# Kernel tuning notes

Measured on AMD Instinct MI355X. Metric: run time of the kernel, lower is better.

## Reference

```python
import jax, jax.numpy as jnp
import numpy as np

SEQ, BATCH, HID, NLAYERS = 2048, 16, 1024, 2


def setup_inputs() -> dict:
    key = jax.random.key(0)
    ks = jax.random.split(key, 3)
    scale = 1.0 / np.sqrt(HID)
    x = jax.random.normal(ks[0], (SEQ, BATCH, HID), dtype=jnp.float32)
    W0 = jax.random.normal(ks[1], (HID, 3 * HID), dtype=jnp.float32) * scale
    b0 = jnp.zeros((2 * HID,), dtype=jnp.float32)
    W1 = jax.random.normal(ks[2], (HID, 3 * HID), dtype=jnp.float32) * scale
    b1 = jnp.zeros((2 * HID,), dtype=jnp.float32)
    return {"x": x, "W0": W0, "b0": b0, "W1": W1, "b1": b1}


def _sru_layer(x, W, b):
    # x: [L, B, H]; W: [H, 3H]; b: [2H]
    L, B, H = x.shape
    U = jnp.einsum('lbd,dk->lbk', x, W)  # [L, B, 3H]
    x_tilde = U[..., :H]
    bf, br = b[:H], b[H:]
    f = jax.nn.sigmoid(U[..., H:2 * H] + bf)  # forget gate [L,B,H]
    r = jax.nn.sigmoid(U[..., 2 * H:] + br)   # reset gate  [L,B,H]

    def step(c_prev, inp):
        xt_t, f_t = inp
        c_t = f_t * c_prev + (1.0 - f_t) * xt_t
        return c_t, c_t

    c0 = jnp.zeros((B, H), dtype=x.dtype)
    _, cs = jax.lax.scan(step, c0, (x_tilde, f))  # cs: [L, B, H]
    h = r * cs + (1.0 - r) * x  # highway connection
    return h


def reference(x, W0, b0, W1, b1):
    h = _sru_layer(x, W0, b0)
    h = _sru_layer(h, W1, b1)
    return h[-1:]  # [1, B, H], matching `out[-1:]`
```

## Files before the change

kernel.cpp:

```cpp
#include <hip/hip_runtime.h>

#define SEQ    2048
#define BATCH  16
#define HID    1024
#define M_TOT  (SEQ*BATCH)
#define NCH    (BATCH*HID)
#define NCHUNK 64
#define TCHUNK (SEQ/NCHUNK)
#define NSEG   256

typedef __attribute__((ext_vector_type(8))) short          short8;
typedef __attribute__((ext_vector_type(8))) unsigned short ushort8_t;
typedef __attribute__((ext_vector_type(4))) float          floatx4;

__device__ __forceinline__ unsigned short f32_to_bf16(float f) {
  unsigned int u = __float_as_uint(f);
  u += 0x7FFFu + ((u >> 16) & 1u);
  return (unsigned short)(u >> 16);
}
__device__ __forceinline__ float bf16_to_f32(unsigned short h) {
  return __uint_as_float(((unsigned int)h) << 16);
}
__device__ __forceinline__ float sigmoidf_(float x) {
  return 1.f / (1.f + __expf(-x));
}


__device__ __forceinline__ void cast_swizzle_body(const float* __restrict__ src,
    unsigned short* __restrict__ dst, int mt, int kt, int t) {
  __shared__ unsigned short tile[4096];
  const int r = t >> 1, kh = (t & 1) * 16;
  const float* sp = src + (size_t)(mt * 128 + r) * 1024 + kt * 32 + kh;
  float4 v0 = *(const float4*)(sp + 0);
  float4 v1 = *(const float4*)(sp + 4);
  float4 v2 = *(const float4*)(sp + 8);
  float4 v3 = *(const float4*)(sp + 12);
  ushort8_t u0, u1;
  u0[0]=f32_to_bf16(v0.x); u0[1]=f32_to_bf16(v0.y); u0[2]=f32_to_bf16(v0.z); u0[3]=f32_to_bf16(v0.w);
  u0[4]=f32_to_bf16(v1.x); u0[5]=f32_to_bf16(v1.y); u0[6]=f32_to_bf16(v1.z); u0[7]=f32_to_bf16(v1.w);
  u1[0]=f32_to_bf16(v2.x); u1[1]=f32_to_bf16(v2.y); u1[2]=f32_to_bf16(v2.z); u1[3]=f32_to_bf16(v2.w);
  u1[4]=f32_to_bf16(v3.x); u1[5]=f32_to_bf16(v3.y); u1[6]=f32_to_bf16(v3.z); u1[7]=f32_to_bf16(v3.w);
  const int c = r >> 4, lr = r & 15, q0 = kh >> 3;
  const int unit0 = c * 64 + (q0 << 4) + lr;
  *(ushort8_t*)&tile[unit0 * 8]        = u0;
  *(ushort8_t*)&tile[(unit0 + 16) * 8] = u1;
  __syncthreads();
  const size_t base = ((size_t)mt * 32 + kt) * 4096;
  *(ushort8_t*)&dst[base + t * 16]     = *(const ushort8_t*)&tile[t * 16];
  *(ushort8_t*)&dst[base + t * 16 + 8] = *(const ushort8_t*)&tile[t * 16 + 8];
}

__device__ __forceinline__ void w_prep_body(const float* __restrict__ W,
    unsigned short* __restrict__ Wsw, int nt, int kt, int t) {
  __shared__ unsigned short tile[4096];
  const int kk = t >> 3, n0 = (t & 7) * 16;
  const float* sp = W + (size_t)(kt * 32 + kk) * 3072 + nt * 128 + n0;
  float v[16];
#pragma unroll
  for (int i = 0; i < 16; i += 4) {
    float4 f = *(const float4*)(sp + i);
    v[i] = f.x; v[i+1] = f.y; v[i+2] = f.z; v[i+3] = f.w;
  }
  const int cbase = (n0 >> 4) * 64 + ((kk >> 3) << 4);
#pragma unroll
  for (int j = 0; j < 16; j++)
    tile[(cbase + j) * 8 + (kk & 7)] = f32_to_bf16(v[j]);
  __syncthreads();
  const size_t base = ((size_t)nt * 32 + kt) * 4096;
  *(ushort8_t*)&Wsw[base + t * 16]     = *(const ushort8_t*)&tile[t * 16];
  *(ushort8_t*)&Wsw[base + t * 16 + 8] = *(const ushort8_t*)&tile[t * 16 + 8];
}

__global__ __launch_bounds__(256) void prep_all(const float* __restrict__ x,
    const float* __restrict__ W0, const float* __restrict__ W1,
    unsigned short* __restrict__ xsw, unsigned short* __restrict__ W0sw,
    unsigned short* __restrict__ W1sw) {
  const int id = blockIdx.x, t = threadIdx.x;
  if (id < 8192)        cast_swizzle_body(x, xsw, id >> 5, id & 31, t);
  else if (id < 8960)   w_prep_body(W0, W0sw, (id - 8192) >> 5, (id - 8192) & 31, t);
  else                  w_prep_body(W1, W1sw, (id - 8960) >> 5, (id - 8960) & 31, t);
}

typedef __attribute__((address_space(1))) const unsigned int GUI;
typedef __attribute__((address_space(3))) unsigned int LUI;
__device__ __forceinline__ void gl16(const unsigned short* g, unsigned short* l) {
  __builtin_amdgcn_global_load_lds((GUI*)g, (LUI*)l, 16, 0, 0);
}
__device__ __forceinline__ void barrier_fence() {
  asm volatile("s_barrier" ::: "memory");
}

__global__ __launch_bounds__(512, 2) void gemm_pipe(
    const unsigned short* __restrict__ A, const unsigned short* __restrict__ B,
    unsigned short* __restrict__ Xt, unsigned short* __restrict__ Fo,
    unsigned short* __restrict__ Ro, const float* __restrict__ bias)
{
  __shared__ unsigned short lds[65536];
  const int tid = threadIdx.x;
  const int wave = tid >> 6, lane = tid & 63;
  const int wm = wave >> 2, wn = wave & 3;
  const int id = blockIdx.x;
  const int xcd = id & 7, slot = id >> 3;
  const int g = slot / 96, r = slot % 96;
  const int bn = r >> 3;
  const int bm = xcd * 16 + g * 8 + (r & 7);

  const unsigned short* aSrc0 = A + ((size_t)(2 * bm + 0) * 32) * 4096 + tid * 8;
  const unsigned short* aSrc1 = A + ((size_t)(2 * bm + 1) * 32) * 4096 + tid * 8;
  const unsigned short* bSrc0 = B + ((size_t)(2 * bn + 0) * 32) * 4096 + tid * 8;
  const unsigned short* bSrc1 = B + ((size_t)(2 * bn + 1) * 32) * 4096 + tid * 8;

  floatx4 acc[8][4];
#pragma unroll
  for (int i = 0; i < 8; i++)
#pragma unroll
    for (int j = 0; j < 4; j++)
#pragma unroll
      for (int rr = 0; rr < 4; rr++) acc[i][j][rr] = 0.f;

#pragma unroll
  for (int u = 0; u < 3; ++u) {
    unsigned short* d = &lds[u * 16384 + wave * 512];
    gl16(aSrc0 + (size_t)u * 4096, d);
    gl16(aSrc1 + (size_t)u * 4096, d + 4096);
    gl16(bSrc0 + (size_t)u * 4096, d + 8192);
    gl16(bSrc1 + (size_t)u * 4096, d + 12288);
  }
  asm volatile("s_waitcnt vmcnt(0)" ::: "memory");
  barrier_fence();

  const int aoff = wm * 4096 + lane * 8;
  const int boff = 8192 + (wn >> 1) * 4096 + (wn & 1) * 2048 + lane * 8;

#pragma unroll 1
  for (int t = 0; t < 32; ++t) {
    const int sb = (t & 3) * 16384;
    const int u = t + 3;
    const unsigned short* As = &lds[sb + aoff];
    const unsigned short* Bs = &lds[sb + boff];
    short8 br[4], ar[4];
#pragma unroll
    for (int nj = 0; nj < 4; ++nj) br[nj] = *(const short8*)(Bs + nj * 512);
#pragma unroll
    for (int mi = 0; mi < 4; ++mi) ar[mi] = *(const short8*)(As + mi * 512);
    if (u < 32) {
      unsigned short* d = &lds[(u & 3) * 16384 + wave * 512];
      gl16(aSrc0 + (size_t)u * 4096, d);
      gl16(aSrc1 + (size_t)u * 4096, d + 4096);
    }
    __builtin_amdgcn_s_setprio(1);
#pragma unroll
    for (int mi = 0; mi < 4; ++mi)
#pragma unroll
      for (int nj = 0; nj < 4; ++nj)
        acc[mi][nj] = __builtin_amdgcn_mfma_f32_16x16x32_bf16(ar[mi], br[nj], acc[mi][nj], 0, 0, 0);
    __builtin_amdgcn_s_setprio(0);
#pragma unroll
    for (int mi = 0; mi < 4; ++mi) ar[mi] = *(const short8*)(As + (4 + mi) * 512);
    if (u < 32) {
      unsigned short* d = &lds[(u & 3) * 16384 + 8192 + wave * 512];
      gl16(bSrc0 + (size_t)u * 4096, d);
      gl16(bSrc1 + (size_t)u * 4096, d + 4096);
    }
    __builtin_amdgcn_s_setprio(1);
#pragma unroll
    for (int mi = 0; mi < 4; ++mi)
#pragma unroll
      for (int nj = 0; nj < 4; ++nj)
        acc[4 + mi][nj] = __builtin_amdgcn_mfma_f32_16x16x32_bf16(ar[mi], br[nj], acc[4 + mi][nj], 0, 0, 0);
    __builtin_amdgcn_s_setprio(0);
    if (t <= 28)      asm volatile("s_waitcnt vmcnt(8)" ::: "memory");
    else if (t == 29) asm volatile("s_waitcnt vmcnt(4)" ::: "memory");
    else if (t == 30) asm volatile("s_waitcnt vmcnt(0)" ::: "memory");
    barrier_fence();
  }

  const int region = bn >> 2;
  const int cc = lane & 15, q = lane >> 4;
  const int lc0 = (bn & 3) * 256 + wn * 64 + cc;
  const int row0 = bm * 256 + wm * 128 + q * 4;
  if (region == 0) {
#pragma unroll
    for (int mi = 0; mi < 8; ++mi)
#pragma unroll
      for (int rg = 0; rg < 4; ++rg)
#pragma unroll
        for (int nj = 0; nj < 4; ++nj)
          Xt[(size_t)(row0 + mi * 16 + rg) * 1024 + lc0 + nj * 16] =
              f32_to_bf16(acc[mi][nj][rg]);
  } else {
    unsigned short* O = (region == 1) ? Fo : Ro;
    const float* bp = bias + (region - 1) * 1024;
    float bb[4];
#pragma unroll
    for (int nj = 0; nj < 4; ++nj) bb[nj] = bp[lc0 + nj * 16];
#pragma unroll
    for (int mi = 0; mi < 8; ++mi)
#pragma unroll
      for (int rg = 0; rg < 4; ++rg)
#pragma unroll
        for (int nj = 0; nj < 4; ++nj) {
          float s = sigmoidf_(acc[mi][nj][rg] + bb[nj]);
          O[(size_t)(row0 + mi * 16 + rg) * 1024 + lc0 + nj * 16] = f32_to_bf16(s);
        }
  }
}

__global__ __launch_bounds__(256, 2) void gemm2_scan(
    const unsigned short* __restrict__ A, const unsigned short* __restrict__ B,
    const float* __restrict__ bias, float* __restrict__ Pseg, float* __restrict__ Sseg)
{
  __shared__ float lps[2][64][4][4][2];
  const int tid = threadIdx.x;
  const int wave = tid >> 6, lane = tid & 63;
  const int wm = wave & 1, wn = wave >> 1;
  const int id = blockIdx.x;
  const int xcd = id & 7, slot = id >> 3;
  const int g = slot >> 6, rem = slot & 63;
  const int bn = rem >> 3;
  const int bm = xcd * 32 + g * 8 + (rem & 7);

  const unsigned short* gA  = A + (size_t)bm * 32 * 4096 + wm * 2048 + lane * 8;
  const unsigned short* gBx = B + (size_t)bn * 32 * 4096 + wn * 2048 + lane * 8;
  const unsigned short* gBf = B + (size_t)(8 + bn) * 32 * 4096 + wn * 2048 + lane * 8;

  floatx4 ax[4][4], af[4][4];
#pragma unroll
  for (int i = 0; i < 4; i++)
#pragma unroll
    for (int j = 0; j < 4; j++)
#pragma unroll
      for (int r = 0; r < 4; r++) { ax[i][j][r] = 0.f; af[i][j][r] = 0.f; }

  short8 a0[4], bx0[4], bf0[4], a1[4], bx1[4], bf1[4];
  auto load4 = [&](short8* d, const unsigned short* p) {
#pragma unroll
    for (int i = 0; i < 4; i++) d[i] = *(const short8*)(p + i * 512);
  };
  auto domfma = [&](short8* a, short8* bx, short8* bf) {
#pragma unroll
    for (int i = 0; i < 4; i++)
#pragma unroll
      for (int j = 0; j < 4; j++) {
        ax[i][j] = __builtin_amdgcn_mfma_f32_16x16x32_bf16(a[i], bx[j], ax[i][j], 0, 0, 0);
        af[i][j] = __builtin_amdgcn_mfma_f32_16x16x32_bf16(a[i], bf[j], af[i][j], 0, 0, 0);
      }
  };

  load4(a0, gA); load4(bx0, gBx); load4(bf0, gBf);
#pragma unroll 1
  for (int kt = 0; kt < 32; kt += 2) {
    load4(a1, gA + 4096); load4(bx1, gBx + 4096); load4(bf1, gBf + 4096);
    domfma(a0, bx0, bf0);
    gA += 8192; gBx += 8192; gBf += 8192;
    if (kt + 2 < 32) { load4(a0, gA); load4(bx0, gBx); load4(bf0, gBf); }
    domfma(a1, bx1, bf1);
  }

  const int q = lane >> 4, cc = lane & 15;
  float pv[4][4], sv[4][4];
#pragma unroll
  for (int j = 0; j < 4; j++) {
    float bb = bias[bn * 128 + wn * 64 + j * 16 + cc];
#pragma unroll
    for (int rg = 0; rg < 4; rg++) {
      float p = 1.f, s = 0.f;
#pragma unroll
      for (int i = 0; i < 4; i++) {
        float f  = sigmoidf_(af[i][j][rg] + bb);
        float xt = ax[i][j][rg];
        s = f * s + (1.f - f) * xt;
        p *= f;
      }
      pv[j][rg] = p; sv[j][rg] = s;
    }
  }
  if (wm == 0) {
#pragma unroll
    for (int j = 0; j < 4; j++)
#pragma unroll
      for (int rg = 0; rg < 4; rg++) {
        lps[wn][lane][rg][j][0] = pv[j][rg];
        lps[wn][lane][rg][j][1] = sv[j][rg];
      }
  }
  __syncthreads();
  if (wm == 1) {
#pragma unroll
    for (int j = 0; j < 4; j++) {
      const int h = bn * 128 + wn * 64 + j * 16 + cc;
#pragma unroll
      for (int rg = 0; rg < 4; rg++) {
        float plo = lps[wn][lane][rg][j][0];
        float slo = lps[wn][lane][rg][j][1];
        float phi = pv[j][rg], shi = sv[j][rg];
        const size_t off = (size_t)bm * NCH + (q * 4 + rg) * 1024 + h;
        Pseg[off] = plo * phi;
        Sseg[off] = phi * slo + shi;
      }
    }
  }
}

__global__ __launch_bounds__(256) void scan_pass1(
    const unsigned short* __restrict__ Xt, const unsigned short* __restrict__ F,
    float* __restrict__ P, float* __restrict__ S) {
  const int ch = (blockIdx.x * 256 + threadIdx.x) * 8;
  const int chunk = blockIdx.y;
  size_t idx = (size_t)chunk * TCHUNK * NCH + ch;
  float p[8], s[8];
#pragma unroll
  for (int j = 0; j < 8; j++) { p[j] = 1.f; s[j] = 0.f; }
  for (int t = 0; t < TCHUNK; ++t) {
    ushort8_t fv = *(const ushort8_t*)&F[idx];
    ushort8_t xv = *(const ushort8_t*)&Xt[idx];
#pragma unroll
    for (int j = 0; j < 8; j++) {
      float f  = bf16_to_f32(fv[j]);
      float xt = bf16_to_f32(xv[j]);
      s[j] = f * s[j] + (1.f - f) * xt;
      p[j] *= f;
    }
    idx += NCH;
  }
  float4* P4 = (float4*)&P[(size_t)chunk * NCH + ch];
  float4* S4 = (float4*)&S[(size_t)chunk * NCH + ch];
  P4[0] = make_float4(p[0], p[1], p[2], p[3]);
  P4[1] = make_float4(p[4], p[5], p[6], p[7]);
  S4[0] = make_float4(s[0], s[1], s[2], s[3]);
  S4[1] = make_float4(s[4], s[5], s[6], s[7]);
}

__global__ __launch_bounds__(256) void combine_c0(
    const float* __restrict__ P, const float* __restrict__ S, float* __restrict__ C0) {
  const int ch = blockIdx.x * 256 + threadIdx.x;
  float c = 0.f;
#pragma unroll 4
  for (int k = 0; k < NCHUNK; ++k) {
    C0[(size_t)k * NCH + ch] = c;
    c = P[(size_t)k * NCH + ch] * c + S[(size_t)k * NCH + ch];
  }
}

#define TPAD 4112
__global__ __launch_bounds__(256) void scan1_pass2_fused(
    const unsigned short* __restrict__ Xt, const unsigned short* __restrict__ F,
    const unsigned short* __restrict__ R, unsigned short* __restrict__ xsw,
    const float* __restrict__ C0, unsigned short* __restrict__ h1last)
{
  __shared__ unsigned short st[4 * TPAD];
  const int hb = blockIdx.x;
  const int chunk = blockIdx.y;
  const int tid = threadIdx.x;
  const int b = tid >> 4, hg = tid & 15;
  const int h0 = hb * 128 + hg * 8;
  const int ch = b * 1024 + h0;
  const int tl   = hg >> 2;
  const int usub = (hg & 3) * 16 + b;

  float c[8];
  {
    const float4* C4 = (const float4*)&C0[(size_t)chunk * NCH + ch];
    float4 a = C4[0], d = C4[1];
    c[0]=a.x; c[1]=a.y; c[2]=a.z; c[3]=a.w; c[4]=d.x; c[5]=d.y; c[6]=d.z; c[7]=d.w;
  }

  size_t idx = (size_t)chunk * TCHUNK * NCH + ch;
  for (int t8 = 0; t8 < TCHUNK / 8; ++t8) {
#pragma unroll
    for (int ts = 0; ts < 8; ++ts) {
      const int t = chunk * TCHUNK + t8 * 8 + ts;
      ushort8_t fv = *(const ushort8_t*)&F[idx];
      ushort8_t xv = *(const ushort8_t*)&Xt[idx];
      ushort8_t rv = *(const ushort8_t*)&R[idx];
      const size_t soff = ((size_t)(t >> 3) * 32 + (h0 >> 5)) * 4096
                        + (size_t)(((t & 7) * 64 + usub) * 8);
      ushort8_t xo = *(const ushort8_t*)&xsw[soff];
      ushort8_t hv;
#pragma unroll
      for (int j = 0; j < 8; ++j) {
        float f  = bf16_to_f32(fv[j]);
        float xt = bf16_to_f32(xv[j]);
        c[j] = f * c[j] + (1.f - f) * xt;
        float r  = bf16_to_f32(rv[j]);
        float xval = bf16_to_f32(xo[j]);
        hv[j] = f32_to_bf16(r * c[j] + (1.f - r) * xval);
      }
      *(ushort8_t*)&st[tl * TPAD + (ts * 64 + usub) * 8] = hv;
      if (t == SEQ - 1) *(ushort8_t*)&h1last[ch] = hv;
      idx += NCH;
    }
    __syncthreads();
    const size_t gbase = (((size_t)chunk * (TCHUNK / 8) + t8) * 32 + hb * 4) * 4096;
#pragma unroll
    for (int tl2 = 0; tl2 < 4; ++tl2) {
      size_t gdst = gbase + (size_t)tl2 * 4096 + tid * 16;
      *(ushort8_t*)&xsw[gdst]     = *(const ushort8_t*)&st[tl2 * TPAD + tid * 16];
      *(ushort8_t*)&xsw[gdst + 8] = *(const ushort8_t*)&st[tl2 * TPAD + tid * 16 + 8];
    }
    __syncthreads();
  }
}

__global__ __launch_bounds__(256) void r2_kernel(
    const unsigned short* __restrict__ h1last, const float* __restrict__ W1,
    const float* __restrict__ b1, float* __restrict__ r2) {
  __shared__ float xrow[1024];
  const int b = blockIdx.x, nq = blockIdx.y, tid = threadIdx.x;
  for (int i = tid; i < 1024; i += 256)
    xrow[i] = bf16_to_f32(h1last[b * 1024 + i]);
  __syncthreads();
  const int n = nq * 256 + tid;
  float acc = b1[1024 + n];
  for (int d = 0; d < 1024; ++d)
    acc += xrow[d] * W1[(size_t)d * 3072 + 2048 + n];
  r2[b * 1024 + n] = sigmoidf_(acc);
}

__global__ __launch_bounds__(256) void final_l2(
    const float* __restrict__ Pseg, const float* __restrict__ Sseg,
    const float* __restrict__ r2, const unsigned short* __restrict__ h1last,
    float* __restrict__ out) {
  const int ch = blockIdx.x * 256 + threadIdx.x;
  float c = 0.f;
#pragma unroll 8
  for (int k = 0; k < NSEG; ++k)
    c = Pseg[(size_t)k * NCH + ch] * c + Sseg[(size_t)k * NCH + ch];
  float r = r2[ch];
  float x = bf16_to_f32(h1last[ch]);
  out[ch] = r * c + (1.f - r) * x;
}

extern "C" void kernel_launch(void* const* d_in, const int* in_sizes, int n_in,
                              void* d_out, int out_size, void* d_ws, size_t ws_size,
                              hipStream_t stream) {
  const float* x  = (const float*)d_in[0];
  const float* W0 = (const float*)d_in[1];
  const float* b0 = (const float*)d_in[2];
  const float* W1 = (const float*)d_in[3];
  const float* b1 = (const float*)d_in[4];
  float* out = (float*)d_out;

  char* ws = (char*)d_ws;
  auto alloc = [&](size_t bytes) {
    char* p = ws; ws += (bytes + 255) & ~(size_t)255; return p;
  };
  const size_t NE = (size_t)M_TOT * HID;
  unsigned short* xsw   = (unsigned short*)alloc(NE * 2);
  unsigned short* W0sw  = (unsigned short*)alloc((size_t)3072 * 1024 * 2);
  unsigned short* W1sw  = (unsigned short*)alloc((size_t)3072 * 1024 * 2);
  unsigned short* Xt    = (unsigned short*)alloc(NE * 2);
  unsigned short* F     = (unsigned short*)alloc(NE * 2);
  unsigned short* R     = (unsigned short*)alloc(NE * 2);
  unsigned short* h1last= (unsigned short*)alloc((size_t)NCH * 2);
  float* P    = (float*)alloc((size_t)NCHUNK * NCH * 4);
  float* S    = (float*)alloc((size_t)NCHUNK * NCH * 4);
  float* C0   = (float*)alloc((size_t)NCHUNK * NCH * 4);
  float* Pseg = (float*)alloc((size_t)NSEG * NCH * 4);
  float* Sseg = (float*)alloc((size_t)NSEG * NCH * 4);
  float* r2   = (float*)alloc((size_t)NCH * 4);

  dim3 blk256(256);
  prep_all<<<dim3(9728), blk256, 0, stream>>>(x, W0, W1, xsw, W0sw, W1sw);
  gemm_pipe<<<dim3(1536), dim3(512), 0, stream>>>(xsw, W0sw, Xt, F, R, b0);
  scan_pass1<<<dim3(8, NCHUNK), blk256, 0, stream>>>(Xt, F, P, S);
  combine_c0<<<dim3(NCH / 256), blk256, 0, stream>>>(P, S, C0);
  scan1_pass2_fused<<<dim3(8, NCHUNK), blk256, 0, stream>>>(Xt, F, R, xsw, C0, h1last);
  r2_kernel<<<dim3(16, 4), blk256, 0, stream>>>(h1last, W1, b1, r2);
  gemm2_scan<<<dim3(2048), blk256, 0, stream>>>(xsw, W1sw, b1, Pseg, Sseg);
  final_l2<<<dim3(NCH / 256), blk256, 0, stream>>>(Pseg, Sseg, r2, h1last, out);
}
```

Before: 743.4 us.

## Shrink layer-1 GEMM tile to 256x128 with 4 waves and triple-buffered LDS

The first-layer GEMM block tile goes from 256x256 with 8 waves to 256x128 with 4 waves, so twice as many blocks are launched. The LDS ring shrinks from four stages of 32 KB to three stages of 24 KB, with prefetch depth two and adjusted waitcnt values. Smaller blocks and less LDS per block should allow more resident blocks and better load balance across CUs. In exchange, each block reuses its A tile across fewer columns, so A traffic from global/L2 doubles, and the shallower pipeline hides less latency.

```diff
diff --git a/kernel.cpp b/kernel.cpp
--- a/kernel.cpp
+++ b/kernel.cpp
@@ -90,25 +90,24 @@
   asm volatile("s_barrier" ::: "memory");
 }
 
-__global__ __launch_bounds__(512, 2) void gemm_pipe(
+__global__ __launch_bounds__(256, 2) void gemm_pipe(
     const unsigned short* __restrict__ A, const unsigned short* __restrict__ B,
     unsigned short* __restrict__ Xt, unsigned short* __restrict__ Fo,
     unsigned short* __restrict__ Ro, const float* __restrict__ bias)
 {
-  __shared__ unsigned short lds[65536];
+  __shared__ unsigned short lds[36864];
   const int tid = threadIdx.x;
   const int wave = tid >> 6, lane = tid & 63;
-  const int wm = wave >> 2, wn = wave & 3;
+  const int wm = wave >> 1, wn = wave & 1;
   const int id = blockIdx.x;
   const int xcd = id & 7, slot = id >> 3;
-  const int g = slot / 96, r = slot % 96;
+  const int g = slot / 192, r = slot % 192;
   const int bn = r >> 3;
   const int bm = xcd * 16 + g * 8 + (r & 7);
 
-  const unsigned short* aSrc0 = A + ((size_t)(2 * bm + 0) * 32) * 4096 + tid * 8;
-  const unsigned short* aSrc1 = A + ((size_t)(2 * bm + 1) * 32) * 4096 + tid * 8;
-  const unsigned short* bSrc0 = B + ((size_t)(2 * bn + 0) * 32) * 4096 + tid * 8;
-  const unsigned short* bSrc1 = B + ((size_t)(2 * bn + 1) * 32) * 4096 + tid * 8;
+  const unsigned short* aSrc0 = A + ((size_t)(2 * bm + 0) * 32) * 4096;
+  const unsigned short* aSrc1 = A + ((size_t)(2 * bm + 1) * 32) * 4096;
+  const unsigned short* bSrc  = B + ((size_t)bn * 32) * 4096;
 
   floatx4 acc[8][4];
 #pragma unroll
@@ -118,24 +117,30 @@
 #pragma unroll
       for (int rr = 0; rr < 4; rr++) acc[i][j][rr] = 0.f;
 
-#pragma unroll
-  for (int u = 0; u < 3; ++u) {
-    unsigned short* d = &lds[u * 16384 + wave * 512];
-    gl16(aSrc0 + (size_t)u * 4096, d);
-    gl16(aSrc1 + (size_t)u * 4096, d + 4096);
-    gl16(bSrc0 + (size_t)u * 4096, d + 8192);
-    gl16(bSrc1 + (size_t)u * 4096, d + 12288);
-  }
-  asm volatile("s_waitcnt vmcnt(0)" ::: "memory");
+  const int tofs = tid * 8;
+  const int dofs = wave * 512;
+  auto stage_chunk = [&](const unsigned short* src, unsigned short* dst) {
+    gl16(src + tofs,        dst + dofs);
+    gl16(src + 2048 + tofs, dst + 2048 + dofs);
+  };
+
+#pragma unroll
+  for (int u = 0; u < 2; ++u) {
+    unsigned short* sl = &lds[u * 12288];
+    stage_chunk(aSrc0 + (size_t)u * 4096, sl);
+    stage_chunk(aSrc1 + (size_t)u * 4096, sl + 4096);
+    stage_chunk(bSrc  + (size_t)u * 4096, sl + 8192);
+  }
+  asm volatile("s_waitcnt vmcnt(6)" ::: "memory");
   barrier_fence();
 
   const int aoff = wm * 4096 + lane * 8;
-  const int boff = 8192 + (wn >> 1) * 4096 + (wn & 1) * 2048 + lane * 8;
-
+  const int boff = 8192 + wn * 2048 + lane * 8;
+
+  int sc = 0, ss = 2;
 #pragma unroll 1
   for (int t = 0; t < 32; ++t) {
-    const int sb = (t & 3) * 16384;
-    const int u = t + 3;
+    const int sb = sc * 12288;
     const unsigned short* As = &lds[sb + aoff];
     const unsigned short* Bs = &lds[sb + boff];
     short8 br[4], ar[4];
@@ -143,10 +148,10 @@
     for (int nj = 0; nj < 4; ++nj) br[nj] = *(const short8*)(Bs + nj * 512);
 #pragma unroll
     for (int mi = 0; mi < 4; ++mi) ar[mi] = *(const short8*)(As + mi * 512);
-    if (u < 32) {
-      unsigned short* d = &lds[(u & 3) * 16384 + wave * 512];
-      gl16(aSrc0 + (size_t)u * 4096, d);
-      gl16(aSrc1 + (size_t)u * 4096, d + 4096);
+    if (t < 30) {
+      unsigned short* sl = &lds[ss * 12288];
+      stage_chunk(aSrc0 + (size_t)(t + 2) * 4096, sl);
+      stage_chunk(aSrc1 + (size_t)(t + 2) * 4096, sl + 4096);
     }
     __builtin_amdgcn_s_setprio(1);
 #pragma unroll
@@ -157,10 +162,9 @@
     __builtin_amdgcn_s_setprio(0);
 #pragma unroll
     for (int mi = 0; mi < 4; ++mi) ar[mi] = *(const short8*)(As + (4 + mi) * 512);
-    if (u < 32) {
-      unsigned short* d = &lds[(u & 3) * 16384 + 8192 + wave * 512];
-      gl16(bSrc0 + (size_t)u * 4096, d);
-      gl16(bSrc1 + (size_t)u * 4096, d + 4096);
+    if (t < 30) {
+      unsigned short* sl = &lds[ss * 12288];
+      stage_chunk(bSrc + (size_t)(t + 2) * 4096, sl + 8192);
     }
     __builtin_amdgcn_s_setprio(1);
 #pragma unroll
@@ -169,15 +173,16 @@
       for (int nj = 0; nj < 4; ++nj)
         acc[4 + mi][nj] = __builtin_amdgcn_mfma_f32_16x16x32_bf16(ar[mi], br[nj], acc[4 + mi][nj], 0, 0, 0);
     __builtin_amdgcn_s_setprio(0);
-    if (t <= 28)      asm volatile("s_waitcnt vmcnt(8)" ::: "memory");
-    else if (t == 29) asm volatile("s_waitcnt vmcnt(4)" ::: "memory");
+    if (t < 30)       asm volatile("s_waitcnt vmcnt(6)" ::: "memory");
     else if (t == 30) asm volatile("s_waitcnt vmcnt(0)" ::: "memory");
     barrier_fence();
-  }
-
-  const int region = bn >> 2;
+    sc = (sc == 2) ? 0 : sc + 1;
+    ss = (ss == 2) ? 0 : ss + 1;
+  }
+
+  const int region = bn >> 3;
   const int cc = lane & 15, q = lane >> 4;
-  const int lc0 = (bn & 3) * 256 + wn * 64 + cc;
+  const int lc0 = (bn & 7) * 128 + wn * 64 + cc;
   const int row0 = bm * 256 + wm * 128 + q * 4;
   if (region == 0) {
 #pragma unroll
@@ -462,7 +467,7 @@
 
   dim3 blk256(256);
   prep_all<<<dim3(9728), blk256, 0, stream>>>(x, W0, W1, xsw, W0sw, W1sw);
-  gemm_pipe<<<dim3(1536), dim3(512), 0, stream>>>(xsw, W0sw, Xt, F, R, b0);
+  gemm_pipe<<<dim3(3072), blk256, 0, stream>>>(xsw, W0sw, Xt, F, R, b0);
   scan_pass1<<<dim3(8, NCHUNK), blk256, 0, stream>>>(Xt, F, P, S);
   combine_c0<<<dim3(NCH / 256), blk256, 0, stream>>>(P, S, C0);
   scan1_pass2_fused<<<dim3(8, NCHUNK), blk256, 0, stream>>>(Xt, F, R, xsw, C0, h1last);
```

Measured after the change: 735.8 us. Within noise of the previous version (-1.0%).

## Rewrite layer-2 GEMM+scan kernel with LDS-staged 4-stage pipeline and larger tiles

Applied to the files above, without the earlier changes.

The second-layer fused GEMM+segment-scan kernel moves from direct global-to-register loads with 256-thread blocks to the 512-thread LDS-staged, 4-buffer pipelined scheme already used by the first GEMM. Each block now covers 256 rows, so the number of scan segments halves (NSEG 256→128) and the Pseg/Sseg traffic into the final kernel drops. This is meant to raise operand reuse and hide global latency. The cost is more LDS use per block, more accumulators per wave, and a longer serial in-block scan over 8 sub-tiles.

```diff
diff --git a/kernel.cpp b/kernel.cpp
--- a/kernel.cpp
+++ b/kernel.cpp
@@ -7,7 +7,7 @@
 #define NCH    (BATCH*HID)
 #define NCHUNK 64
 #define TCHUNK (SEQ/NCHUNK)
-#define NSEG   256
+#define NSEG   128
 
 typedef __attribute__((ext_vector_type(8))) short          short8;
 typedef __attribute__((ext_vector_type(8))) unsigned short ushort8_t;
@@ -158,9 +158,9 @@
 #pragma unroll
     for (int mi = 0; mi < 4; ++mi) ar[mi] = *(const short8*)(As + (4 + mi) * 512);
     if (u < 32) {
-      unsigned short* d = &lds[(u & 3) * 16384 + 8192 + wave * 512];
-      gl16(bSrc0 + (size_t)u * 4096, d);
-      gl16(bSrc1 + (size_t)u * 4096, d + 4096);
+      unsigned short* d = &lds[(u & 3) * 16384 + wave * 512];
+      gl16(bSrc0 + (size_t)u * 4096, d + 8192);
+      gl16(bSrc1 + (size_t)u * 4096, d + 12288);
     }
     __builtin_amdgcn_s_setprio(1);
 #pragma unroll
@@ -206,94 +206,138 @@
   }
 }
 
-__global__ __launch_bounds__(256, 2) void gemm2_scan(
+__global__ __launch_bounds__(512, 2) void gemm2_scan(
     const unsigned short* __restrict__ A, const unsigned short* __restrict__ B,
     const float* __restrict__ bias, float* __restrict__ Pseg, float* __restrict__ Sseg)
 {
-  __shared__ float lps[2][64][4][4][2];
+  __shared__ unsigned short lds[65536];
   const int tid = threadIdx.x;
   const int wave = tid >> 6, lane = tid & 63;
-  const int wm = wave & 1, wn = wave >> 1;
+  const int wm = wave >> 2, wn = wave & 3;
   const int id = blockIdx.x;
   const int xcd = id & 7, slot = id >> 3;
-  const int g = slot >> 6, rem = slot & 63;
-  const int bn = rem >> 3;
-  const int bm = xcd * 32 + g * 8 + (rem & 7);
-
-  const unsigned short* gA  = A + (size_t)bm * 32 * 4096 + wm * 2048 + lane * 8;
-  const unsigned short* gBx = B + (size_t)bn * 32 * 4096 + wn * 2048 + lane * 8;
-  const unsigned short* gBf = B + (size_t)(8 + bn) * 32 * 4096 + wn * 2048 + lane * 8;
-
-  floatx4 ax[4][4], af[4][4];
-#pragma unroll
-  for (int i = 0; i < 4; i++)
-#pragma unroll
-    for (int j = 0; j < 4; j++)
-#pragma unroll
-      for (int r = 0; r < 4; r++) { ax[i][j][r] = 0.f; af[i][j][r] = 0.f; }
-
-  short8 a0[4], bx0[4], bf0[4], a1[4], bx1[4], bf1[4];
-  auto load4 = [&](short8* d, const unsigned short* p) {
-#pragma unroll
-    for (int i = 0; i < 4; i++) d[i] = *(const short8*)(p + i * 512);
-  };
-  auto domfma = [&](short8* a, short8* bx, short8* bf) {
-#pragma unroll
-    for (int i = 0; i < 4; i++)
-#pragma unroll
-      for (int j = 0; j < 4; j++) {
-        ax[i][j] = __builtin_amdgcn_mfma_f32_16x16x32_bf16(a[i], bx[j], ax[i][j], 0, 0, 0);
-        af[i][j] = __builtin_amdgcn_mfma_f32_16x16x32_bf16(a[i], bf[j], af[i][j], 0, 0, 0);
+  const int bn = slot >> 4;
+  const int bm = xcd * 16 + (slot & 15);
+
+  const unsigned short* aSrc0 = A + ((size_t)(2 * bm + 0) * 32) * 4096 + tid * 8;
+  const unsigned short* aSrc1 = A + ((size_t)(2 * bm + 1) * 32) * 4096 + tid * 8;
+  const unsigned short* bxSrc = B + ((size_t)bn * 32) * 4096 + tid * 8;
+  const unsigned short* bfSrc = B + ((size_t)(8 + bn) * 32) * 4096 + tid * 8;
+
+  floatx4 ax[8][2], af[8][2];
+#pragma unroll
+  for (int i = 0; i < 8; i++)
+#pragma unroll
+    for (int j = 0; j < 2; j++)
+#pragma unroll
+      for (int rr = 0; rr < 4; rr++) { ax[i][j][rr] = 0.f; af[i][j][rr] = 0.f; }
+
+#pragma unroll
+  for (int u = 0; u < 3; ++u) {
+    unsigned short* d = &lds[u * 16384 + wave * 512];
+    gl16(aSrc0 + (size_t)u * 4096, d);
+    gl16(aSrc1 + (size_t)u * 4096, d + 4096);
+    gl16(bxSrc + (size_t)u * 4096, d + 8192);
+    gl16(bfSrc + (size_t)u * 4096, d + 12288);
+  }
+  asm volatile("s_waitcnt vmcnt(0)" ::: "memory");
+  barrier_fence();
+
+  const int aoff  = wm * 4096 + lane * 8;
+  const int bxoff = 8192  + wn * 1024 + lane * 8;
+  const int bfoff = 12288 + wn * 1024 + lane * 8;
+
+#pragma unroll 1
+  for (int t = 0; t < 32; ++t) {
+    const int sb = (t & 3) * 16384;
+    const int u = t + 3;
+    const unsigned short* As  = &lds[sb + aoff];
+    const unsigned short* Bxs = &lds[sb + bxoff];
+    const unsigned short* Bfs = &lds[sb + bfoff];
+    short8 bx[2], bf[2], ar[4];
+#pragma unroll
+    for (int nj = 0; nj < 2; ++nj) {
+      bx[nj] = *(const short8*)(Bxs + nj * 512);
+      bf[nj] = *(const short8*)(Bfs + nj * 512);
+    }
+#pragma unroll
+    for (int mi = 0; mi < 4; ++mi) ar[mi] = *(const short8*)(As + mi * 512);
+    if (u < 32) {
+      unsigned short* d = &lds[(u & 3) * 16384 + wave * 512];
+      gl16(aSrc0 + (size_t)u * 4096, d);
+      gl16(aSrc1 + (size_t)u * 4096, d + 4096);
+    }
+    __builtin_amdgcn_s_setprio(1);
+#pragma unroll
+    for (int mi = 0; mi < 4; ++mi)
+#pragma unroll
+      for (int nj = 0; nj < 2; ++nj) {
+        ax[mi][nj] = __builtin_amdgcn_mfma_f32_16x16x32_bf16(ar[mi], bx[nj], ax[mi][nj], 0, 0, 0);
+        af[mi][nj] = __builtin_amdgcn_mfma_f32_16x16x32_bf16(ar[mi], bf[nj], af[mi][nj], 0, 0, 0);
       }
-  };
-
-  load4(a0, gA); load4(bx0, gBx); load4(bf0, gBf);
-#pragma unroll 1
-  for (int kt = 0; kt < 32; kt += 2) {
-    load4(a1, gA + 4096); load4(bx1, gBx + 4096); load4(bf1, gBf + 4096);
-    domfma(a0, bx0, bf0);
-    gA += 8192; gBx += 8192; gBf += 8192;
-    if (kt + 2 < 32) { load4(a0, gA); load4(bx0, gBx); load4(bf0, gBf); }
-    domfma(a1, bx1, bf1);
+    __builtin_amdgcn_s_setprio(0);
+#pragma unroll
+    for (int mi = 0; mi < 4; ++mi) ar[mi] = *(const short8*)(As + (4 + mi) * 512);
+    if (u < 32) {
+      unsigned short* d = &lds[(u & 3) * 16384 + wave * 512];
+      gl16(bxSrc + (size_t)u * 4096, d + 8192);
+      gl16(bfSrc + (size_t)u * 4096, d + 12288);
+    }
+    __builtin_amdgcn_s_setprio(1);
+#pragma unroll
+    for (int mi = 0; mi < 4; ++mi)
+#pragma unroll
+      for (int nj = 0; nj < 2; ++nj) {
+        ax[4 + mi][nj] = __builtin_amdgcn_mfma_f32_16x16x32_bf16(ar[mi], bx[nj], ax[4 + mi][nj], 0, 0, 0);
+        af[4 + mi][nj] = __builtin_amdgcn_mfma_f32_16x16x32_bf16(ar[mi], bf[nj], af[4 + mi][nj], 0, 0, 0);
+      }
+    __builtin_amdgcn_s_setprio(0);
+    if (t <= 28)      asm volatile("s_waitcnt vmcnt(8)" ::: "memory");
+    else if (t == 29) asm volatile("s_waitcnt vmcnt(4)" ::: "memory");
+    else if (t == 30) asm volatile("s_waitcnt vmcnt(0)" ::: "memory");
+    barrier_fence();
   }
 
   const int q = lane >> 4, cc = lane & 15;
-  float pv[4][4], sv[4][4];
-#pragma unroll
-  for (int j = 0; j < 4; j++) {
-    float bb = bias[bn * 128 + wn * 64 + j * 16 + cc];
-#pragma unroll
-    for (int rg = 0; rg < 4; rg++) {
+  float pv[2][4], sv[2][4];
+#pragma unroll
+  for (int nj = 0; nj < 2; ++nj) {
+    float bb = bias[bn * 128 + wn * 32 + nj * 16 + cc];
+#pragma unroll
+    for (int rg = 0; rg < 4; ++rg) {
       float p = 1.f, s = 0.f;
 #pragma unroll
-      for (int i = 0; i < 4; i++) {
-        float f  = sigmoidf_(af[i][j][rg] + bb);
-        float xt = ax[i][j][rg];
+      for (int mi = 0; mi < 8; ++mi) {
+        float f  = sigmoidf_(af[mi][nj][rg] + bb);
+        float xt = ax[mi][nj][rg];
         s = f * s + (1.f - f) * xt;
         p *= f;
       }
-      pv[j][rg] = p; sv[j][rg] = s;
-    }
-  }
+      pv[nj][rg] = p; sv[nj][rg] = s;
+    }
+  }
+  float* lf = (float*)lds;
+  __syncthreads();
   if (wm == 0) {
 #pragma unroll
-    for (int j = 0; j < 4; j++)
-#pragma unroll
-      for (int rg = 0; rg < 4; rg++) {
-        lps[wn][lane][rg][j][0] = pv[j][rg];
-        lps[wn][lane][rg][j][1] = sv[j][rg];
+    for (int nj = 0; nj < 2; ++nj)
+#pragma unroll
+      for (int rg = 0; rg < 4; ++rg) {
+        const int idx = (((wn * 64 + lane) * 4 + rg) * 2 + nj) * 2;
+        lf[idx]     = pv[nj][rg];
+        lf[idx + 1] = sv[nj][rg];
       }
   }
   __syncthreads();
   if (wm == 1) {
 #pragma unroll
-    for (int j = 0; j < 4; j++) {
-      const int h = bn * 128 + wn * 64 + j * 16 + cc;
-#pragma unroll
-      for (int rg = 0; rg < 4; rg++) {
-        float plo = lps[wn][lane][rg][j][0];
-        float slo = lps[wn][lane][rg][j][1];
-        float phi = pv[j][rg], shi = sv[j][rg];
+    for (int nj = 0; nj < 2; ++nj) {
+      const int h = bn * 128 + wn * 32 + nj * 16 + cc;
+#pragma unroll
+      for (int rg = 0; rg < 4; ++rg) {
+        const int idx = (((wn * 64 + lane) * 4 + rg) * 2 + nj) * 2;
+        float plo = lf[idx], slo = lf[idx + 1];
+        float phi = pv[nj][rg], shi = sv[nj][rg];
         const size_t off = (size_t)bm * NCH + (q * 4 + rg) * 1024 + h;
         Pseg[off] = plo * phi;
         Sseg[off] = phi * slo + shi;
@@ -467,6 +511,6 @@
   combine_c0<<<dim3(NCH / 256), blk256, 0, stream>>>(P, S, C0);
   scan1_pass2_fused<<<dim3(8, NCHUNK), blk256, 0, stream>>>(Xt, F, R, xsw, C0, h1last);
   r2_kernel<<<dim3(16, 4), blk256, 0, stream>>>(h1last, W1, b1, r2);
-  gemm2_scan<<<dim3(2048), blk256, 0, stream>>>(xsw, W1sw, b1, Pseg, Sseg);
+  gemm2_scan<<<dim3(1024), dim3(512), 0, stream>>>(xsw, W1sw, b1, Pseg, Sseg);
   final_l2<<<dim3(NCH / 256), blk256, 0, stream>>>(Pseg, Sseg, r2, h1last, out);
 }
```

Measured after the change: 731.6 us. About the same (-1.6%).
